# Kernel optimization log

Measured on AMD Instinct MI355X. Metric: run time of the kernel, lower is better.

## Reference

```python
import jax, jax.numpy as jnp
import numpy as np

D = 1024
H = 16
K = D // H
B = 2
S = 2048

def setup_inputs() -> dict:
    key = jax.random.key(0)
    k1, k2, k3, k4, k5 = jax.random.split(key, 5)
    x = jax.random.normal(k1, (B, S, D), dtype=jnp.float32)
    # nn.Linear(d, 3d): weight [3d, d], bias [3d]
    Wqkv = jax.random.normal(k2, (3 * D, D), dtype=jnp.float32) / np.sqrt(D)
    bqkv = jax.random.normal(k3, (3 * D,), dtype=jnp.float32) * 0.01
    Wproj = jax.random.normal(k4, (D, D), dtype=jnp.float32) / np.sqrt(D)
    bproj = jax.random.normal(k5, (D,), dtype=jnp.float32) * 0.01
    return {"x": x, "Wqkv": Wqkv, "bqkv": bqkv, "Wproj": Wproj, "bproj": bproj}

def reference(x, Wqkv, bqkv, Wproj, bproj):
    Bsz, Slen, d = x.shape
    # fused QKV projection: [B,S,3d] -> [B,S,3,H,K] -> (3, B, H, S, K)
    qkv = (jnp.einsum('bsd,ed->bse', x, Wqkv) + bqkv).reshape(Bsz, Slen, 3, H, K)
    q, k, v = jnp.moveaxis(qkv, 2, 0).transpose(0, 1, 3, 2, 4)
    scale = 1.0 / jnp.sqrt(jnp.asarray(K, dtype=x.dtype))
    scores = jnp.einsum('bhqk,bhmk->bhqm', q, k) * scale  # [B,H,S,S]
    a = jax.nn.softmax(scores, axis=-1)
    # dropout is identity in eval mode
    o = jnp.einsum('bhqm,bhmk->bhqk', a, v)  # [B,H,S,K]
    o = o.transpose(0, 2, 1, 3).reshape(Bsz, Slen, d)
    return jnp.einsum('bsd,ed->bse', o, Wproj) + bproj
```

## Files before the change

### kernel.cpp

```cpp
#include <hip/hip_runtime.h>
#include <cstdint>

typedef unsigned short ushort_t;
typedef short short8 __attribute__((ext_vector_type(8)));
typedef float f32x4 __attribute__((ext_vector_type(4)));
typedef float float4v __attribute__((ext_vector_type(4)));
typedef unsigned int uint2v __attribute__((ext_vector_type(2)));

#define DDIM 1024
#define HH 16
#define HEADK 64
#define BB 2
#define SS 2048

#if __has_builtin(__builtin_amdgcn_exp2f)
#define EXP2F(x) __builtin_amdgcn_exp2f(x)
#else
#define EXP2F(x) exp2f(x)
#endif

__device__ __forceinline__ ushort_t f2bf(float f) {
  union { float f; uint32_t u; } c; c.f = f;
  uint32_t u = c.u;
  u += 0x7fffu + ((u >> 16) & 1u);
  return (ushort_t)(u >> 16);
}

__device__ __forceinline__ uint32_t pkbf_trunc(float a, float b) {
  union { float f; uint32_t u; } ca, cb;
  ca.f = a; cb.f = b;
  return __builtin_amdgcn_perm(cb.u, ca.u, 0x07060302);
}

__device__ __forceinline__ uint32_t pkbf_rne(float a, float b) {
  return (uint32_t)f2bf(a) | ((uint32_t)f2bf(b) << 16);
}

__device__ __forceinline__ float bfhi2f(uint32_t u) {
  union { uint32_t u; float f; } c; c.u = u & 0xffff0000u; return c.f;
}
__device__ __forceinline__ float bflo2f(uint32_t u) {
  union { uint32_t u; float f; } c; c.u = u << 16; return c.f;
}

__device__ __forceinline__ void glds16(const ushort_t* gp, ushort_t* lp) {
  __builtin_amdgcn_global_load_lds(
      (const __attribute__((address_space(1))) uint32_t*)gp,
      (__attribute__((address_space(3))) uint32_t*)lp, 16, 0, 0);
}

__global__ void cvt3_kernel(const float* __restrict__ s0, ushort_t* __restrict__ d0, int n0,
                            const float* __restrict__ s1, ushort_t* __restrict__ d1, int n1,
                            const float* __restrict__ s2, ushort_t* __restrict__ d2, int n2) {
  int i = blockIdx.x * blockDim.x + threadIdx.x;
  const float* src; ushort_t* dst; int k;
  if (i < n0) { src = s0; dst = d0; k = i; }
  else if (i < n0 + n1) { src = s1; dst = d1; k = i - n0; }
  else if (i < n0 + n1 + n2) { src = s2; dst = d2; k = i - n0 - n1; }
  else return;
  float4v v = ((const float4v*)src)[k];
  uint2v o; o[0] = pkbf_rne(v[0], v[1]); o[1] = pkbf_rne(v[2], v[3]);
  ((uint2v*)dst)[k] = o;
}

template <int MODE, int TM>
__global__ __launch_bounds__(256) void gemm_nt(
    const ushort_t* __restrict__ A, const ushort_t* __restrict__ Bm,
    const float* __restrict__ bias, float* __restrict__ Cout,
    ushort_t* __restrict__ Cbf, int M, int N, int Kd) {
  __shared__ ushort_t smem[128 * 64 * 2];
  ushort_t* As = smem;
  ushort_t* Bs = smem + TM * 64;
  const int MI = TM / 32;
  const int tid = threadIdx.x;
  const int wv = tid >> 6, lane = tid & 63;
  const int l15 = lane & 15, quad = lane >> 4;
  const int wm = wv >> 1, wn = wv & 1;
  const int tm0 = blockIdx.y * TM, tn0 = blockIdx.x * 128;

  f32x4 acc[MI][4];
#pragma unroll
  for (int i = 0; i < MI; ++i)
#pragma unroll
    for (int j = 0; j < 4; ++j) acc[i][j] = (f32x4){0.f, 0.f, 0.f, 0.f};

  const int lrow = lane >> 3;
  const int gcb = (lane & 7) ^ lrow;
  const int ACI = TM / 32;

  for (int k0 = 0; k0 < Kd; k0 += 64) {
#pragma unroll
    for (int c = 0; c < ACI; ++c) {
      int seg = wv * ACI + c;
      glds16(A + (size_t)(tm0 + seg * 8 + lrow) * Kd + k0 + gcb * 8,
             As + seg * 512);
    }
#pragma unroll
    for (int c = 0; c < 4; ++c) {
      int seg = wv * 4 + c;
      glds16(Bm + (size_t)(tn0 + seg * 8 + lrow) * Kd + k0 + gcb * 8,
             Bs + seg * 512);
    }
    __syncthreads();
#pragma unroll
    for (int kk = 0; kk < 64; kk += 32) {
      short8 af[MI], bfr[4];
#pragma unroll
      for (int i = 0; i < MI; ++i) {
        int r = wm * (TM / 2) + i * 16 + l15;
        int cb = (kk >> 3) + quad;
        af[i] = *(const short8*)(As + r * 64 + ((cb ^ (l15 & 7)) << 3));
      }
#pragma unroll
      for (int j = 0; j < 4; ++j) {
        int r = wn * 64 + j * 16 + l15;
        int cb = (kk >> 3) + quad;
        bfr[j] = *(const short8*)(Bs + r * 64 + ((cb ^ (l15 & 7)) << 3));
      }
#pragma unroll
      for (int i = 0; i < MI; ++i)
#pragma unroll
        for (int j = 0; j < 4; ++j)
          acc[i][j] = __builtin_amdgcn_mfma_f32_16x16x32_bf16(
              af[i], bfr[j], acc[i][j], 0, 0, 0);
    }
    __syncthreads();
  }

  if (MODE == 1) {
#pragma unroll
    for (int j = 0; j < 4; ++j) {
      int col = tn0 + wn * 64 + j * 16 + l15;
      float bv = bias[col];
#pragma unroll
      for (int i = 0; i < MI; ++i) {
        int row0 = tm0 + wm * (TM / 2) + i * 16 + quad * 4;
#pragma unroll
        for (int r = 0; r < 4; ++r)
          Cout[(size_t)(row0 + r) * N + col] = acc[i][j][r] + bv;
      }
    }
  } else {
    const int t = tn0 >> 10;
    if (t < 2) {
#pragma unroll
      for (int j = 0; j < 4; ++j) {
        int col = tn0 + wn * 64 + j * 16 + l15;
        float bv = bias[col];
        int hh = (col >> 6) & 15, kk2 = col & 63;
#pragma unroll
        for (int i = 0; i < MI; ++i) {
          int row0 = tm0 + wm * (TM / 2) + i * 16 + quad * 4;
#pragma unroll
          for (int r = 0; r < 4; ++r) {
            int row = row0 + r;
            int b = row >> 11, s = row & 2047;
            float v = acc[i][j][r] + bv;
            if (t == 0) v *= 0.18033688f;
            size_t base =
                (((size_t)t * BB + b) * HH + hh) * ((size_t)SS * HEADK);
            Cbf[base + (size_t)s * HEADK + kk2] = f2bf(v);
          }
        }
      }
    } else {
      __syncthreads();
#pragma unroll
      for (int j = 0; j < 4; ++j) {
        int c = wn * 64 + j * 16 + l15;
        float bv = bias[tn0 + c];
#pragma unroll
        for (int i = 0; i < MI; ++i) {
          int row0 = wm * (TM / 2) + i * 16 + quad * 4;
          uint2v dw;
          dw[0] = pkbf_rne(acc[i][j][0] + bv, acc[i][j][1] + bv);
          dw[1] = pkbf_rne(acc[i][j][2] + bv, acc[i][j][3] + bv);
          int rb = row0 >> 3;
          *(uint2v*)(&smem[c * 128 + (((rb ^ (c & 15)) << 3) | (row0 & 7))]) =
              dw;
        }
      }
      __syncthreads();
      const int rb2 = lane & 15;
      const int cg = lane >> 4;
#pragma unroll
      for (int it = 0; it < 8; ++it) {
        int c = wv * 32 + it * 4 + cg;
        short8 vv = *(const short8*)(&smem[c * 128 + ((rb2 ^ (c & 15)) << 3)]);
        int gcol = tn0 + c;
        int hh = (gcol >> 6) & 15, kk2 = gcol & 63;
        int grow = tm0 + rb2 * 8;
        int b = grow >> 11, s = grow & 2047;
        size_t base = (((size_t)2 * BB + b) * HH + hh) * ((size_t)SS * HEADK);
        *(short8*)(&Cbf[base + (size_t)kk2 * SS + s]) = vv;
      }
    }
  }
}

__global__ __launch_bounds__(256, 4) void attn_kernel(
    const ushort_t* __restrict__ qkv, ushort_t* __restrict__ Op0,
    ushort_t* __restrict__ Op1, float* __restrict__ Lp) {
  __shared__ ushort_t Kt[2][32 * 64];
  __shared__ ushort_t Vt[2][64 * 32];
  __shared__ ushort_t Pw[4][32 * 32];

  const int qt = blockIdx.x, h = blockIdx.y;
  const int b = blockIdx.z >> 1, ns = blockIdx.z & 1;
  const int tid = threadIdx.x;
  const int wv = tid >> 6, lane = tid & 63;
  const int l15 = lane & 15, quad = lane >> 4;

  const size_t hstride = (size_t)SS * HEADK;
  const ushort_t* Qg = qkv + ((size_t)(0 * BB + b) * HH + h) * hstride;
  const ushort_t* Kg = qkv + ((size_t)(1 * BB + b) * HH + h) * hstride;
  const ushort_t* Vg = qkv + ((size_t)(2 * BB + b) * HH + h) * hstride;
  ushort_t* Opp = ns ? Op1 : Op0;

  short8 qf[2][2];
#pragma unroll
  for (int mi = 0; mi < 2; ++mi)
#pragma unroll
    for (int kc = 0; kc < 2; ++kc)
      qf[mi][kc] = *(const short8*)(
          Qg + (size_t)(qt * 128 + wv * 32 + mi * 16 + l15) * 64 + kc * 32 +
          quad * 8);

  const short ONE = (short)0x3F80;
  short8 ones = {ONE, ONE, ONE, ONE, ONE, ONE, ONE, ONE};

  f32x4 oat[2][4];
  f32x4 loa[2];
#pragma unroll
  for (int mi = 0; mi < 2; ++mi) {
    loa[mi] = (f32x4){0.f, 0.f, 0.f, 0.f};
#pragma unroll
    for (int c = 0; c < 4; ++c) oat[mi][c] = (f32x4){0.f, 0.f, 0.f, 0.f};
  }

  const int lrow = lane >> 3, gcb = (lane & 7) ^ lrow;
  const int vfl = lane >> 2;
  const int vgb = (lane & 3) ^ ((vfl >> 1) & 3);

  const int pos0 = ns * (SS / 2);

  auto stage = [&](int jj, int db) {
    glds16(Kg + (size_t)(pos0 + jj * 32 + wv * 8 + lrow) * 64 + gcb * 8,
           &Kt[db][wv * 512]);
    glds16(Vg + (size_t)(wv * 16 + vfl) * SS + pos0 + jj * 32 + vgb * 8,
           &Vt[db][wv * 512]);
  };

  stage(0, 0);

  for (int j = 0; j < 32; ++j) {
    const int db = j & 1;
    __syncthreads();
    if (j + 1 < 32) stage(j + 1, db ^ 1);

    f32x4 st[2][2];
#pragma unroll
    for (int cf = 0; cf < 2; ++cf) {
      int n = cf * 16 + l15;
      short8 kf0 = *(const short8*)(&Kt[db][n * 64 + ((quad ^ (n & 7)) << 3)]);
      short8 kf1 =
          *(const short8*)(&Kt[db][n * 64 + (((quad + 4) ^ (n & 7)) << 3)]);
#pragma unroll
      for (int mi = 0; mi < 2; ++mi) {
        f32x4 z = (f32x4){0.f, 0.f, 0.f, 0.f};
        z = __builtin_amdgcn_mfma_f32_16x16x32_bf16(kf0, qf[mi][0], z, 0, 0, 0);
        z = __builtin_amdgcn_mfma_f32_16x16x32_bf16(kf1, qf[mi][1], z, 0, 0, 0);
        st[mi][cf] = z;
      }
    }

#pragma unroll
    for (int mi = 0; mi < 2; ++mi)
#pragma unroll
      for (int cf = 0; cf < 2; ++cf) {
        float e0 = EXP2F(st[mi][cf][0]);
        float e1 = EXP2F(st[mi][cf][1]);
        float e2 = EXP2F(st[mi][cf][2]);
        float e3 = EXP2F(st[mi][cf][3]);
        uint2v dw;
        dw[0] = pkbf_trunc(e0, e1);
        dw[1] = pkbf_trunc(e2, e3);
        int row = mi * 16 + l15;
        int pb = 2 * cf + (quad >> 1);
        int pbs = pb ^ ((l15 >> 1) & 3);
        *(uint2v*)(&Pw[wv][row * 32 + pbs * 8 + (quad & 1) * 4]) = dw;
      }

    short8 pa[2];
#pragma unroll
    for (int mi = 0; mi < 2; ++mi) {
      int row = mi * 16 + l15;
      pa[mi] = *(const short8*)(&Pw[wv][row * 32 +
                                        ((quad ^ ((l15 >> 1) & 3)) << 3)]);
    }

#pragma unroll
    for (int cf = 0; cf < 4; ++cf) {
      short8 vf = *(const short8*)(&Vt[db][(cf * 16 + l15) * 32 +
                                           ((quad ^ ((l15 >> 1) & 3)) << 3)]);
#pragma unroll
      for (int mi = 0; mi < 2; ++mi)
        oat[mi][cf] = __builtin_amdgcn_mfma_f32_16x16x32_bf16(
            vf, pa[mi], oat[mi][cf], 0, 0, 0);
    }
#pragma unroll
    for (int mi = 0; mi < 2; ++mi)
      loa[mi] = __builtin_amdgcn_mfma_f32_16x16x32_bf16(ones, pa[mi], loa[mi],
                                                        0, 0, 0);
  }

  const size_t obase = ((size_t)b * HH + h) * SS * HEADK;
#pragma unroll
  for (int mi = 0; mi < 2; ++mi) {
#pragma unroll
    for (int cf = 0; cf < 4; ++cf) {
      uint2v dw;
      dw[0] = pkbf_rne(oat[mi][cf][0], oat[mi][cf][1]);
      dw[1] = pkbf_rne(oat[mi][cf][2], oat[mi][cf][3]);
      int cb = 2 * cf + (quad >> 1);
      int cbs = cb ^ (l15 & 7);
      *(uint2v*)(&Pw[wv][l15 * 64 + cbs * 8 + (quad & 1) * 4]) = dw;
    }
    const int r = lane >> 2;
#pragma unroll
    for (int pass = 0; pass < 2; ++pass) {
      int g = (lane & 3) + 4 * pass;
      short8 ov = *(const short8*)(&Pw[wv][r * 64 + ((g ^ (r & 7)) << 3)]);
      int qrow = qt * 128 + wv * 32 + mi * 16 + r;
      *(short8*)(&Opp[obase + (size_t)qrow * 64 + g * 8]) = ov;
    }
    if (quad == 0) {
      int qrow = qt * 128 + wv * 32 + mi * 16 + l15;
      Lp[((size_t)(ns * BB + b) * HH + h) * SS + qrow] = loa[mi][0];
    }
  }
}

__global__ void reduce_kernel(const ushort_t* __restrict__ Op0,
                              const ushort_t* __restrict__ Op1,
                              const float* __restrict__ Lp,
                              ushort_t* __restrict__ ob) {
  const size_t nsL = (size_t)BB * HH * SS;
  int c = blockIdx.x * blockDim.x + threadIdx.x;
  int fc = c & 7;
  int hh = (c >> 3) & 15;
  int row = c >> 7;
  int b = row >> 11, s = row & 2047;
  size_t po = (((size_t)b * HH + hh) * SS + s) * 64 + fc * 8;
  uint2v a0 = *(const uint2v*)(&Op0[po]);
  uint2v a1 = *(const uint2v*)(&Op0[po + 4]);
  uint2v b0 = *(const uint2v*)(&Op1[po]);
  uint2v b1 = *(const uint2v*)(&Op1[po + 4]);
  size_t lo = ((size_t)b * HH + hh) * SS + s;
  float inv = 1.0f / (Lp[lo] + Lp[nsL + lo]);
  uint2v o0, o1;
  o0[0] = pkbf_rne((bflo2f(a0[0]) + bflo2f(b0[0])) * inv,
                   (bfhi2f(a0[0]) + bfhi2f(b0[0])) * inv);
  o0[1] = pkbf_rne((bflo2f(a0[1]) + bflo2f(b0[1])) * inv,
                   (bfhi2f(a0[1]) + bfhi2f(b0[1])) * inv);
  o1[0] = pkbf_rne((bflo2f(a1[0]) + bflo2f(b1[0])) * inv,
                   (bfhi2f(a1[0]) + bfhi2f(b1[0])) * inv);
  o1[1] = pkbf_rne((bflo2f(a1[1]) + bflo2f(b1[1])) * inv,
                   (bfhi2f(a1[1]) + bfhi2f(b1[1])) * inv);
  size_t oo = ((size_t)(b * SS + s)) * DDIM + hh * 64 + fc * 8;
  *(uint2v*)(&ob[oo]) = o0;
  *(uint2v*)(&ob[oo + 4]) = o1;
}

extern "C" void kernel_launch(void* const* d_in, const int* in_sizes, int n_in,
                              void* d_out, int out_size, void* d_ws,
                              size_t ws_size, hipStream_t stream) {
  const float* x = (const float*)d_in[0];
  const float* Wqkv = (const float*)d_in[1];
  const float* bqkv = (const float*)d_in[2];
  const float* Wproj = (const float*)d_in[3];
  const float* bproj = (const float*)d_in[4];
  float* out = (float*)d_out;

  ushort_t* xb = (ushort_t*)d_ws;
  ushort_t* wqb = xb + (size_t)4096 * 1024;
  ushort_t* wpb = wqb + (size_t)3072 * 1024;
  ushort_t* qkvb = wpb + (size_t)1024 * 1024;
  ushort_t* Op1 = qkvb + (size_t)3 * BB * HH * SS * HEADK;
  ushort_t* Op0 = xb;
  float* Lp = (float*)wqb;
  ushort_t* obuf = qkvb;

  const int n0 = 4096 * 1024 / 4, n1 = 3072 * 1024 / 4, n2 = 1024 * 1024 / 4;
  cvt3_kernel<<<(n0 + n1 + n2 + 255) / 256, 256, 0, stream>>>(
      x, xb, n0, Wqkv, wqb, n1, Wproj, wpb, n2);
  gemm_nt<0, 128><<<dim3(3072 / 128, 4096 / 128), 256, 0, stream>>>(
      xb, wqb, bqkv, nullptr, qkvb, 4096, 3072, 1024);
  attn_kernel<<<dim3(16, 16, 4), 256, 0, stream>>>(qkvb, Op0, Op1, Lp);
  reduce_kernel<<<(BB * SS * DDIM / 8) / 256, 256, 0, stream>>>(Op0, Op1, Lp,
                                                                obuf);
  gemm_nt<1, 64><<<dim3(1024 / 128, 4096 / 64), 256, 0, stream>>>(
      obuf, wpb, bproj, out, nullptr, 4096, 1024, 1024);
}
```

Measured before the change: 193.9 us.

## Split attention KV range four ways and triple-buffer K/V staging with setprio

The attention kernel is templated on the number of KV splits and uses four splits when the workspace is large enough, doubling the grid. Each split writes its own partial output buffer, and the reduce kernel sums four partials. The K/V shared-memory staging goes from double to triple buffering with explicit vmcnt waits and raw barriers, so two tiles are in flight at once. MFMA sections are wrapped in s_setprio to favour matrix issue. The cost is more partial-output traffic in the reduce, extra LDS per block, and a launch path that depends on the workspace size.

```diff
diff --git a/kernel.cpp b/kernel.cpp
--- a/kernel.cpp
+++ b/kernel.cpp
@@ -198,15 +198,18 @@
   }
 }
 
+template <int NSPLIT>
 __global__ __launch_bounds__(256, 4) void attn_kernel(
-    const ushort_t* __restrict__ qkv, ushort_t* __restrict__ Op0,
-    ushort_t* __restrict__ Op1, float* __restrict__ Lp) {
-  __shared__ ushort_t Kt[2][32 * 64];
-  __shared__ ushort_t Vt[2][64 * 32];
+    const ushort_t* __restrict__ qkv, ushort_t* __restrict__ O0,
+    ushort_t* __restrict__ O1, ushort_t* __restrict__ O2,
+    ushort_t* __restrict__ O3, float* __restrict__ Lp) {
+  constexpr int NT = (SS / NSPLIT) / 32;
+  __shared__ ushort_t Kt[3][32 * 64];
+  __shared__ ushort_t Vt[3][64 * 32];
   __shared__ ushort_t Pw[4][32 * 32];
 
   const int qt = blockIdx.x, h = blockIdx.y;
-  const int b = blockIdx.z >> 1, ns = blockIdx.z & 1;
+  const int b = blockIdx.z / NSPLIT, ns = blockIdx.z % NSPLIT;
   const int tid = threadIdx.x;
   const int wv = tid >> 6, lane = tid & 63;
   const int l15 = lane & 15, quad = lane >> 4;
@@ -215,7 +218,12 @@
   const ushort_t* Qg = qkv + ((size_t)(0 * BB + b) * HH + h) * hstride;
   const ushort_t* Kg = qkv + ((size_t)(1 * BB + b) * HH + h) * hstride;
   const ushort_t* Vg = qkv + ((size_t)(2 * BB + b) * HH + h) * hstride;
-  ushort_t* Opp = ns ? Op1 : Op0;
+  ushort_t* Opp;
+  if (NSPLIT == 2) {
+    Opp = ns ? O1 : O0;
+  } else {
+    Opp = (ns == 0) ? O0 : (ns == 1) ? O1 : (ns == 2) ? O2 : O3;
+  }
 
   short8 qf[2][2];
 #pragma unroll
@@ -242,7 +250,7 @@
   const int vfl = lane >> 2;
   const int vgb = (lane & 3) ^ ((vfl >> 1) & 3);
 
-  const int pos0 = ns * (SS / 2);
+  const int pos0 = ns * (SS / NSPLIT);
 
   auto stage = [&](int jj, int db) {
     glds16(Kg + (size_t)(pos0 + jj * 32 + wv * 8 + lrow) * 64 + gcb * 8,
@@ -252,19 +260,32 @@
   };
 
   stage(0, 0);
-
-  for (int j = 0; j < 32; ++j) {
-    const int db = j & 1;
-    __syncthreads();
-    if (j + 1 < 32) stage(j + 1, db ^ 1);
+  stage(1, 1);
+
+  int cur = 0;
+  for (int j = 0; j < NT; ++j) {
+    if (j + 1 < NT)
+      asm volatile("s_waitcnt vmcnt(2)" ::: "memory");
+    else
+      asm volatile("s_waitcnt vmcnt(0)" ::: "memory");
+    __builtin_amdgcn_s_barrier();
+    asm volatile("" ::: "memory");
+    __builtin_amdgcn_sched_barrier(0);
+
+    if (j + 2 < NT) {
+      int tgt = cur + 2;
+      if (tgt >= 3) tgt -= 3;
+      stage(j + 2, tgt);
+    }
 
     f32x4 st[2][2];
+    __builtin_amdgcn_s_setprio(1);
 #pragma unroll
     for (int cf = 0; cf < 2; ++cf) {
       int n = cf * 16 + l15;
-      short8 kf0 = *(const short8*)(&Kt[db][n * 64 + ((quad ^ (n & 7)) << 3)]);
+      short8 kf0 = *(const short8*)(&Kt[cur][n * 64 + ((quad ^ (n & 7)) << 3)]);
       short8 kf1 =
-          *(const short8*)(&Kt[db][n * 64 + (((quad + 4) ^ (n & 7)) << 3)]);
+          *(const short8*)(&Kt[cur][n * 64 + (((quad + 4) ^ (n & 7)) << 3)]);
 #pragma unroll
       for (int mi = 0; mi < 2; ++mi) {
         f32x4 z = (f32x4){0.f, 0.f, 0.f, 0.f};
@@ -273,6 +294,7 @@
         st[mi][cf] = z;
       }
     }
+    __builtin_amdgcn_s_setprio(0);
 
 #pragma unroll
     for (int mi = 0; mi < 2; ++mi)
@@ -299,10 +321,11 @@
                                         ((quad ^ ((l15 >> 1) & 3)) << 3)]);
     }
 
+    __builtin_amdgcn_s_setprio(1);
 #pragma unroll
     for (int cf = 0; cf < 4; ++cf) {
-      short8 vf = *(const short8*)(&Vt[db][(cf * 16 + l15) * 32 +
-                                           ((quad ^ ((l15 >> 1) & 3)) << 3)]);
+      short8 vf = *(const short8*)(&Vt[cur][(cf * 16 + l15) * 32 +
+                                            ((quad ^ ((l15 >> 1) & 3)) << 3)]);
 #pragma unroll
       for (int mi = 0; mi < 2; ++mi)
         oat[mi][cf] = __builtin_amdgcn_mfma_f32_16x16x32_bf16(
@@ -312,6 +335,9 @@
     for (int mi = 0; mi < 2; ++mi)
       loa[mi] = __builtin_amdgcn_mfma_f32_16x16x32_bf16(ones, pa[mi], loa[mi],
                                                         0, 0, 0);
+    __builtin_amdgcn_s_setprio(0);
+
+    cur = (cur == 2) ? 0 : cur + 1;
   }
 
   const size_t obase = ((size_t)b * HH + h) * SS * HEADK;
@@ -341,8 +367,11 @@
   }
 }
 
-__global__ void reduce_kernel(const ushort_t* __restrict__ Op0,
-                              const ushort_t* __restrict__ Op1,
+template <int NSPLIT>
+__global__ void reduce_kernel(const ushort_t* __restrict__ O0,
+                              const ushort_t* __restrict__ O1,
+                              const ushort_t* __restrict__ O2,
+                              const ushort_t* __restrict__ O3,
                               const float* __restrict__ Lp,
                               ushort_t* __restrict__ ob) {
   const size_t nsL = (size_t)BB * HH * SS;
@@ -352,21 +381,28 @@
   int row = c >> 7;
   int b = row >> 11, s = row & 2047;
   size_t po = (((size_t)b * HH + hh) * SS + s) * 64 + fc * 8;
-  uint2v a0 = *(const uint2v*)(&Op0[po]);
-  uint2v a1 = *(const uint2v*)(&Op0[po + 4]);
-  uint2v b0 = *(const uint2v*)(&Op1[po]);
-  uint2v b1 = *(const uint2v*)(&Op1[po + 4]);
   size_t lo = ((size_t)b * HH + hh) * SS + s;
-  float inv = 1.0f / (Lp[lo] + Lp[nsL + lo]);
+  const ushort_t* Ops[4] = {O0, O1, O2, O3};
+  float acc[8];
+#pragma unroll
+  for (int i = 0; i < 8; ++i) acc[i] = 0.f;
+  float l = 0.f;
+#pragma unroll
+  for (int t = 0; t < NSPLIT; ++t) {
+    uint2v a0 = *(const uint2v*)(&Ops[t][po]);
+    uint2v a1 = *(const uint2v*)(&Ops[t][po + 4]);
+    acc[0] += bflo2f(a0[0]); acc[1] += bfhi2f(a0[0]);
+    acc[2] += bflo2f(a0[1]); acc[3] += bfhi2f(a0[1]);
+    acc[4] += bflo2f(a1[0]); acc[5] += bfhi2f(a1[0]);
+    acc[6] += bflo2f(a1[1]); acc[7] += bfhi2f(a1[1]);
+    l += Lp[(size_t)t * nsL + lo];
+  }
+  float inv = 1.0f / l;
   uint2v o0, o1;
-  o0[0] = pkbf_rne((bflo2f(a0[0]) + bflo2f(b0[0])) * inv,
-                   (bfhi2f(a0[0]) + bfhi2f(b0[0])) * inv);
-  o0[1] = pkbf_rne((bflo2f(a0[1]) + bflo2f(b0[1])) * inv,
-                   (bfhi2f(a0[1]) + bfhi2f(b0[1])) * inv);
-  o1[0] = pkbf_rne((bflo2f(a1[0]) + bflo2f(b1[0])) * inv,
-                   (bfhi2f(a1[0]) + bfhi2f(b1[0])) * inv);
-  o1[1] = pkbf_rne((bflo2f(a1[1]) + bflo2f(b1[1])) * inv,
-                   (bfhi2f(a1[1]) + bfhi2f(b1[1])) * inv);
+  o0[0] = pkbf_rne(acc[0] * inv, acc[1] * inv);
+  o0[1] = pkbf_rne(acc[2] * inv, acc[3] * inv);
+  o1[0] = pkbf_rne(acc[4] * inv, acc[5] * inv);
+  o1[1] = pkbf_rne(acc[6] * inv, acc[7] * inv);
   size_t oo = ((size_t)(b * SS + s)) * DDIM + hh * 64 + fc * 8;
   *(uint2v*)(&ob[oo]) = o0;
   *(uint2v*)(&ob[oo + 4]) = o1;
@@ -387,6 +423,8 @@
   ushort_t* wpb = wqb + (size_t)3072 * 1024;
   ushort_t* qkvb = wpb + (size_t)1024 * 1024;
   ushort_t* Op1 = qkvb + (size_t)3 * BB * HH * SS * HEADK;
+  ushort_t* Op2 = Op1 + (size_t)BB * HH * SS * HEADK;
+  ushort_t* Op3 = Op2 + (size_t)BB * HH * SS * HEADK;
   ushort_t* Op0 = xb;
   float* Lp = (float*)wqb;
   ushort_t* obuf = qkvb;
@@ -396,9 +434,19 @@
       x, xb, n0, Wqkv, wqb, n1, Wproj, wpb, n2);
   gemm_nt<0, 128><<<dim3(3072 / 128, 4096 / 128), 256, 0, stream>>>(
       xb, wqb, bqkv, nullptr, qkvb, 4096, 3072, 1024);
-  attn_kernel<<<dim3(16, 16, 4), 256, 0, stream>>>(qkvb, Op0, Op1, Lp);
-  reduce_kernel<<<(BB * SS * DDIM / 8) / 256, 256, 0, stream>>>(Op0, Op1, Lp,
-                                                                obuf);
+
+  const size_t need4 = 67108864ull;
+  if (ws_size >= need4) {
+    attn_kernel<4><<<dim3(16, 16, BB * 4), 256, 0, stream>>>(qkvb, Op0, Op1,
+                                                             Op2, Op3, Lp);
+    reduce_kernel<4><<<(BB * SS * DDIM / 8) / 256, 256, 0, stream>>>(
+        Op0, Op1, Op2, Op3, Lp, obuf);
+  } else {
+    attn_kernel<2><<<dim3(16, 16, BB * 2), 256, 0, stream>>>(qkvb, Op0, Op1,
+                                                             Op1, Op1, Lp);
+    reduce_kernel<2><<<(BB * SS * DDIM / 8) / 256, 256, 0, stream>>>(
+        Op0, Op1, Op1, Op1, Lp, obuf);
+  }
   gemm_nt<1, 64><<<dim3(1024 / 128, 4096 / 64), 256, 0, stream>>>(
       obuf, wpb, bproj, out, nullptr, 4096, 1024, 1024);
 }
```

Result: no change. 195.4 us (+0.8%).
